# Performance work log

Measured on AMD Instinct MI355X. Metric: run time of the kernel, lower is better.

## Reference

```python
import jax, jax.numpy as jnp
import numpy as np

M, N, D = 4, 65536, 256

def setup_inputs() -> dict:
    key = jax.random.key(0)
    k1, k2, k3 = jax.random.split(key, 3)
    x = jax.random.normal(k1, (M, N, D), dtype=jnp.float32)
    # W[i,j] is the (out,in) weight of fusion_layers[i][j]; b[i,j] its bias.
    W = jax.random.normal(k2, (M, M, D, D), dtype=jnp.float32) * (1.0 / np.sqrt(D))
    b = jax.random.normal(k3, (M, M, D), dtype=jnp.float32) * 0.02
    return {"x": x, "W": W, "b": b}

def reference(x, W, b):
    # x: [M, N, D] stacked modality features (zip(*features) rows vectorized over N)
    # out[i] = x[i] + sum_{j != i} (x[j] @ W[i,j]^T + b[i,j])
    m = x.shape[0]
    mask = (1.0 - jnp.eye(m)).astype(x.dtype)            # zero on diagonal (skip i==j)
    y = jnp.einsum('ijef,jnf->ijne', W, x) + b[:, :, None, :]  # [M, M, N, D]
    out = x + jnp.einsum('ij,ijne->ine', mask, y)         # fused masked accumulation
    return out
```

## Files before the change

### kernel.cpp

```cpp
#include <hip/hip_runtime.h>
#include <hip/hip_bf16.h>
#include <stdint.h>

#define NN 65536
#define DD 256

typedef uint32_t u32;
typedef __attribute__((ext_vector_type(4))) float f32x4;
typedef __attribute__((ext_vector_type(4))) u32 u32x4;
typedef __attribute__((ext_vector_type(2))) u32 u32x2;
typedef __attribute__((ext_vector_type(8))) short s16x8;

__device__ inline unsigned short f2bf(float f) {
    union { float f; u32 u; } v; v.f = f;
    u32 u = v.u;
    return (unsigned short)((u + 0x7fffu + ((u >> 16) & 1u)) >> 16);
}

__device__ inline void gl2lds16(const void* g, void* s) {
    __builtin_amdgcn_global_load_lds(
        (const __attribute__((address_space(1))) void*)g,
        (__attribute__((address_space(3))) void*)s, 16, 0, 0);
}

__global__ void prep_w(const float* __restrict__ W, unsigned short* __restrict__ Wimg, int diag) {
    int t = blockIdx.x * blockDim.x + threadIdx.x;
    int E = t * 4;
    int tile = E >> 13;
    int pin = E & 8191;
    int col = pin >> 6;
    int r2e = pin & 63;
    int ct = tile >> 4;
    int j = (tile >> 2) & 3;
    int kk = tile & 3;
    int kl = r2e ^ ((col & 7) << 3);
    int c = ct * 128 + col;
    int i = c >> 8, e = c & 255;
    int f = kk * 64 + kl;
    u32 p0, p1;
    if (i == j) {
        unsigned short d0 = 0, d1 = 0, d2 = 0, d3 = 0;
        if (diag) {
            d0 = (e == f + 0) ? 0x3F80 : 0;
            d1 = (e == f + 1) ? 0x3F80 : 0;
            d2 = (e == f + 2) ? 0x3F80 : 0;
            d3 = (e == f + 3) ? 0x3F80 : 0;
        }
        p0 = (u32)d0 | ((u32)d1 << 16);
        p1 = (u32)d2 | ((u32)d3 << 16);
    } else {
        f32x4 w = *(const f32x4*)(W + ((size_t)((i * 4 + j) * 256 + e) << 8) + f);
        p0 = (u32)f2bf(w[0]) | ((u32)f2bf(w[1]) << 16);
        p1 = (u32)f2bf(w[2]) | ((u32)f2bf(w[3]) << 16);
    }
    u32x2 pr = {p0, p1};
    *(u32x2*)(Wimg + E) = pr;
}

__global__ void prep_x(const float* __restrict__ x, unsigned short* __restrict__ Ximg) {
    int t = blockIdx.x * blockDim.x + threadIdx.x;
    long long E = (long long)t * 4;
    int tile = (int)(E >> 14);
    int pin = (int)(E & 16383);
    int row = pin >> 6;
    int r2e = pin & 63;
    int kk = tile & 3;
    int rt = (tile >> 2) & 255;
    int j = tile >> 10;
    int kl = r2e ^ ((row & 7) << 3);
    int n = rt * 256 + row;
    int f = kk * 64 + kl;
    f32x4 v = *(const f32x4*)(x + ((size_t)j * NN + n) * DD + f);
    u32 p0 = (u32)f2bf(v[0]) | ((u32)f2bf(v[1]) << 16);
    u32 p1 = (u32)f2bf(v[2]) | ((u32)f2bf(v[3]) << 16);
    u32x2 pr = {p0, p1};
    *(u32x2*)(Ximg + E) = pr;
}

__global__ void prep_b(const float* __restrict__ b, float* __restrict__ bsum) {
    int c = blockIdx.x * blockDim.x + threadIdx.x;
    if (c >= 1024) return;
    int i = c >> 8, e = c & 255;
    float s = 0.0f;
    #pragma unroll
    for (int j = 0; j < 4; ++j)
        if (j != i) s += b[((i * 4 + j) << 8) + e];
    bsum[c] = s;
}

__global__ __launch_bounds__(512, 1) void fusion_gemm3(
    const unsigned short* __restrict__ Wimg, const unsigned short* __restrict__ Ximg,
    const float* __restrict__ bsum, float* __restrict__ out) {
    __shared__ __attribute__((aligned(16))) char lds[3][49152];

    const int tid = threadIdx.x;
    const int bid = blockIdx.x;
    const int xcd = bid & 7;
    const int slot = bid >> 3;
    const int ct = slot & 7;
    const int rhi = slot >> 3;
    const int rtile = rhi * 8 + xcd;
    const int n0 = rtile * 256;
    const int col0 = ct * 128;
    const int i = ct >> 1;
    (void)i;

    const int lane = tid & 63;
    const int wid = tid >> 6;
    const int wm = wid >> 1;
    const int wn = wid & 1;

    f32x4 acc[4][4];
    #pragma unroll
    for (int a = 0; a < 4; ++a)
        #pragma unroll
        for (int b2 = 0; b2 < 4; ++b2)
            acc[a][b2] = (f32x4){0.f, 0.f, 0.f, 0.f};

    const char* WimgB = (const char*)Wimg;
    const char* XimgB = (const char*)Ximg;
    const u32 goff = (u32)(wid * 1024 + lane * 16);
    const u32 loff = (u32)(wid * 1024);

#define STAGE(t_, bsel_)                                                              \
    {                                                                                 \
        int j_ = (t_) >> 2;                                                           \
        int kk_ = (t_) & 3;                                                           \
        const char* ab_ = XimgB + (((size_t)(j_ * 256 + rtile) * 4 + kk_) << 15) + goff; \
        char* al_ = lds[bsel_] + loff;                                                \
        _Pragma("unroll")                                                             \
        for (int q = 0; q < 4; ++q) gl2lds16(ab_ + q * 8192, al_ + q * 8192);         \
        const char* bb_ = WimgB + (((size_t)(ct * 4 + j_) * 4 + kk_) << 14) + goff;   \
        char* bl_ = lds[bsel_] + 32768 + loff;                                        \
        _Pragma("unroll")                                                             \
        for (int q = 0; q < 2; ++q) gl2lds16(bb_ + q * 8192, bl_ + q * 8192);         \
    }

#define MFMA_STEP(bsel_)                                                              \
    {                                                                                 \
        const char* Ab_ = lds[bsel_];                                                 \
        const char* Bb_ = lds[bsel_] + 32768;                                         \
        _Pragma("unroll")                                                             \
        for (int kh = 0; kh < 2; ++kh) {                                              \
            s16x8 af[4], bfr[4];                                                      \
            _Pragma("unroll")                                                         \
            for (int fm = 0; fm < 4; ++fm) {                                          \
                int row = wm * 64 + fm * 16 + (lane & 15);                            \
                u32 o = (u32)(row * 128 + kh * 64 + (lane >> 4) * 16);                \
                o ^= (u32)((row & 7) << 4);                                           \
                af[fm] = *(const s16x8*)(Ab_ + o);                                    \
            }                                                                         \
            _Pragma("unroll")                                                         \
            for (int fn = 0; fn < 4; ++fn) {                                          \
                int col = wn * 64 + fn * 16 + (lane & 15);                            \
                u32 o = (u32)(col * 128 + kh * 64 + (lane >> 4) * 16);                \
                o ^= (u32)((col & 7) << 4);                                           \
                bfr[fn] = *(const s16x8*)(Bb_ + o);                                   \
            }                                                                         \
            _Pragma("unroll")                                                         \
            for (int fm = 0; fm < 4; ++fm)                                            \
                _Pragma("unroll")                                                     \
                for (int fn = 0; fn < 4; ++fn)                                        \
                    acc[fm][fn] = __builtin_amdgcn_mfma_f32_16x16x32_bf16(            \
                        af[fm], bfr[fn], acc[fm][fn], 0, 0, 0);                       \
        }                                                                             \
    }

    STAGE(0, 0);
    STAGE(1, 1);

    #pragma unroll 1
    for (int t = 0; t < 14; ++t) {
        asm volatile("s_waitcnt vmcnt(6)" ::: "memory");
        __builtin_amdgcn_s_barrier();
        __builtin_amdgcn_sched_barrier(0);
        STAGE(t + 2, (t + 2) % 3);
        __builtin_amdgcn_s_setprio(1);
        MFMA_STEP(t % 3);
        __builtin_amdgcn_s_setprio(0);
    }
    asm volatile("s_waitcnt vmcnt(6)" ::: "memory");
    __builtin_amdgcn_s_barrier();
    __builtin_amdgcn_sched_barrier(0);
    __builtin_amdgcn_s_setprio(1);
    MFMA_STEP(2);
    __builtin_amdgcn_s_setprio(0);
    asm volatile("s_waitcnt vmcnt(0)" ::: "memory");
    __builtin_amdgcn_s_barrier();
    __builtin_amdgcn_sched_barrier(0);
    __builtin_amdgcn_s_setprio(1);
    MFMA_STEP(0);
    __builtin_amdgcn_s_setprio(0);

#undef STAGE
#undef MFMA_STEP

    const int r0 = (lane >> 4) * 4;
    const int cl = lane & 15;
    const int iout = ct >> 1;
    #pragma unroll
    for (int fm = 0; fm < 4; ++fm) {
        #pragma unroll
        for (int fn = 0; fn < 4; ++fn) {
            int col_l = wn * 64 + fn * 16 + cl;
            int cglob = col0 + col_l;
            float bs = bsum[cglob];
            int e = cglob & 255;
            #pragma unroll
            for (int r = 0; r < 4; ++r) {
                int row_l = wm * 64 + fm * 16 + r0 + r;
                int n = n0 + row_l;
                size_t oidx = ((size_t)iout * NN + n) * DD + e;
                out[oidx] = acc[fm][fn][r] + bs;
            }
        }
    }
}

__global__ __launch_bounds__(256, 2) void fusion_gemm_fb(
    const float* __restrict__ x, const unsigned short* __restrict__ Wimg,
    const float* __restrict__ bsum, float* __restrict__ out) {
    __shared__ __attribute__((aligned(16))) unsigned short Alds[128 * 64];
    __shared__ __attribute__((aligned(16))) unsigned short Blds[2][128 * 64];

    const int tid = threadIdx.x;
    const int bid = blockIdx.x;
    const int xcd = bid & 7;
    const int slot = bid >> 3;
    const int ct = slot & 7;
    const int rhi = slot >> 3;
    const int rtile = rhi * 8 + xcd;
    const int n0 = rtile * 128;
    const int col0 = ct * 128;
    const int i = ct >> 1;

    const int lane = tid & 63;
    const int wid = tid >> 6;
    const int wm = wid >> 1;
    const int wn = wid & 1;

    f32x4 acc[4][4];
    #pragma unroll
    for (int a = 0; a < 4; ++a)
        #pragma unroll
        for (int b2 = 0; b2 < 4; ++b2)
            acc[a][b2] = (f32x4){0.f, 0.f, 0.f, 0.f};

    const int sr = tid >> 1;
    const int sh = tid & 1;
    char* Ab = (char*)Alds;
    const char* WimgB = (const char*)Wimg;

    f32x4 av[8];
    {
        int j0 = (i == 0) ? 1 : 0;
        const float* asrc = x + (size_t)j0 * ((size_t)NN * DD) + (size_t)(n0 + sr) * DD + sh * 32;
        #pragma unroll
        for (int q = 0; q < 8; ++q) av[q] = *(const f32x4*)(asrc + q * 4);
        const char* base = WimgB + (((size_t)(ct * 4 + j0) * 4 + 0) << 14) + wid * 1024 + lane * 16;
        char* lb = (char*)Blds[0] + wid * 1024;
        #pragma unroll
        for (int q = 0; q < 4; ++q) gl2lds16(base + q * 4096, lb + q * 4096);
    }

    for (int t = 0; t < 12; ++t) {
        __syncthreads();
        #pragma unroll
        for (int q = 0; q < 4; ++q) {
            f32x4 v0 = av[2 * q], v1 = av[2 * q + 1];
            u32x4 p;
            p[0] = (u32)f2bf(v0[0]) | ((u32)f2bf(v0[1]) << 16);
            p[1] = (u32)f2bf(v0[2]) | ((u32)f2bf(v0[3]) << 16);
            p[2] = (u32)f2bf(v1[0]) | ((u32)f2bf(v1[1]) << 16);
            p[3] = (u32)f2bf(v1[2]) | ((u32)f2bf(v1[3]) << 16);
            u32 o = (u32)(sr * 128 + sh * 64 + q * 16);
            o ^= (u32)((sr & 7) << 4);
            *(u32x4*)(Ab + o) = p;
        }
        __syncthreads();

        if (t < 11) {
            int tn = t + 1;
            int jjn = tn >> 2;
            int jn = jjn + (jjn >= i);
            int kkn = tn & 3;
            const char* base = WimgB + (((size_t)(ct * 4 + jn) * 4 + kkn) << 14) + wid * 1024 + lane * 16;
            char* lb = (char*)Blds[tn & 1] + wid * 1024;
            #pragma unroll
            for (int q = 0; q < 4; ++q) gl2lds16(base + q * 4096, lb + q * 4096);
            const float* asrc = x + (size_t)jn * ((size_t)NN * DD) + (size_t)(n0 + sr) * DD + kkn * 64 + sh * 32;
            #pragma unroll
            for (int q = 0; q < 8; ++q) av[q] = *(const f32x4*)(asrc + q * 4);
        }

        const char* Bb = (const char*)Blds[t & 1];
        #pragma unroll
        for (int kh = 0; kh < 2; ++kh) {
            s16x8 af[4], bfr[4];
            #pragma unroll
            for (int fm = 0; fm < 4; ++fm) {
                int row = wm * 64 + fm * 16 + (lane & 15);
                u32 o = (u32)(row * 128 + kh * 64 + (lane >> 4) * 16);
                o ^= (u32)((row & 7) << 4);
                af[fm] = *(const s16x8*)(Ab + o);
            }
            #pragma unroll
            for (int fn = 0; fn < 4; ++fn) {
                int col = wn * 64 + fn * 16 + (lane & 15);
                u32 o = (u32)(col * 128 + kh * 64 + (lane >> 4) * 16);
                o ^= (u32)((col & 7) << 4);
                bfr[fn] = *(const s16x8*)(Bb + o);
            }
            #pragma unroll
            for (int fm = 0; fm < 4; ++fm)
                #pragma unroll
                for (int fn = 0; fn < 4; ++fn)
                    acc[fm][fn] = __builtin_amdgcn_mfma_f32_16x16x32_bf16(
                        af[fm], bfr[fn], acc[fm][fn], 0, 0, 0);
        }
    }

    const int r0 = (lane >> 4) * 4;
    const int cl = lane & 15;
    #pragma unroll
    for (int fm = 0; fm < 4; ++fm) {
        #pragma unroll
        for (int fn = 0; fn < 4; ++fn) {
            int col_l = wn * 64 + fn * 16 + cl;
            int cglob = col0 + col_l;
            float bs = bsum[cglob];
            int e = cglob & 255;
            #pragma unroll
            for (int r = 0; r < 4; ++r) {
                int row_l = wm * 64 + fm * 16 + r0 + r;
                int n = n0 + row_l;
                size_t oidx = ((size_t)i * NN + n) * DD + e;
                out[oidx] = acc[fm][fn][r] + x[oidx] + bs;
            }
        }
    }
}

extern "C" void kernel_launch(void* const* d_in, const int* in_sizes, int n_in,
                              void* d_out, int out_size, void* d_ws, size_t ws_size,
                              hipStream_t stream) {
    const float* x = (const float*)d_in[0];
    const float* W = (const float*)d_in[1];
    const float* b = (const float*)d_in[2];
    float* out = (float*)d_out;

    unsigned short* Wimg = (unsigned short*)d_ws;
    float* bsum = (float*)((char*)d_ws + ((size_t)2 << 20));
    const size_t ximg_off = (size_t)4 << 20;
    const size_t need = ximg_off + ((size_t)128 << 20);

    hipLaunchKernelGGL(prep_b, dim3(4), dim3(256), 0, stream, b, bsum);

    if (ws_size >= need) {
        unsigned short* Ximg = (unsigned short*)((char*)d_ws + ximg_off);
        hipLaunchKernelGGL(prep_w, dim3(1024), dim3(256), 0, stream, W, Wimg, 1);
        hipLaunchKernelGGL(prep_x, dim3(65536), dim3(256), 0, stream, x, Ximg);
        hipLaunchKernelGGL(fusion_gemm3, dim3(2048), dim3(512), 0, stream, Wimg, Ximg, bsum, out);
    } else {
        hipLaunchKernelGGL(prep_w, dim3(1024), dim3(256), 0, stream, W, Wimg, 0);
        hipLaunchKernelGGL(fusion_gemm_fb, dim3(4096), dim3(256), 0, stream, x, Wimg, bsum, out);
    }
}
```

Baseline: 262.2 us.

## Enlarge GEMM tile to 256x256 with double-buffered LDS and interleaved quadrant MFMA schedule

The main GEMM tile grows from 256x128 to 256x256 output columns per block, halving the grid and the number of times each X tile is re-read. The weight image is re-laid out to match. The triple-buffered LDS ring becomes a 2x64KB double buffer whose next-stage loads are split into four pieces and interleaved with four MFMA quadrant clusters, each guarded by barriers. Each wave now holds 128 accumulator registers, which raises register pressure, and the launch bound asks for two blocks per CU, which the 128KB of LDS may not permit.

```diff
diff --git a/kernel.cpp b/kernel.cpp
--- a/kernel.cpp
+++ b/kernel.cpp
@@ -23,7 +23,38 @@
         (__attribute__((address_space(3))) void*)s, 16, 0, 0);
 }
 
-__global__ void prep_w(const float* __restrict__ W, unsigned short* __restrict__ Wimg, int diag) {
+__global__ void prep_w256(const float* __restrict__ W, unsigned short* __restrict__ Wimg) {
+    int t = blockIdx.x * blockDim.x + threadIdx.x;
+    int E = t * 4;
+    int tile = E >> 14;
+    int pin = E & 16383;
+    int col = pin >> 6;
+    int r2e = pin & 63;
+    int ct = tile >> 4;
+    int j = (tile >> 2) & 3;
+    int kk = tile & 3;
+    int kl = r2e ^ ((col & 7) << 3);
+    int i = ct;
+    int e = col;
+    int f = kk * 64 + kl;
+    u32 p0, p1;
+    if (i == j) {
+        unsigned short d0 = (e == f + 0) ? 0x3F80 : 0;
+        unsigned short d1 = (e == f + 1) ? 0x3F80 : 0;
+        unsigned short d2 = (e == f + 2) ? 0x3F80 : 0;
+        unsigned short d3 = (e == f + 3) ? 0x3F80 : 0;
+        p0 = (u32)d0 | ((u32)d1 << 16);
+        p1 = (u32)d2 | ((u32)d3 << 16);
+    } else {
+        f32x4 w = *(const f32x4*)(W + ((size_t)((i * 4 + j) * 256 + e) << 8) + f);
+        p0 = (u32)f2bf(w[0]) | ((u32)f2bf(w[1]) << 16);
+        p1 = (u32)f2bf(w[2]) | ((u32)f2bf(w[3]) << 16);
+    }
+    u32x2 pr = {p0, p1};
+    *(u32x2*)(Wimg + E) = pr;
+}
+
+__global__ void prep_w128(const float* __restrict__ W, unsigned short* __restrict__ Wimg) {
     int t = blockIdx.x * blockDim.x + threadIdx.x;
     int E = t * 4;
     int tile = E >> 13;
@@ -39,15 +70,7 @@
     int f = kk * 64 + kl;
     u32 p0, p1;
     if (i == j) {
-        unsigned short d0 = 0, d1 = 0, d2 = 0, d3 = 0;
-        if (diag) {
-            d0 = (e == f + 0) ? 0x3F80 : 0;
-            d1 = (e == f + 1) ? 0x3F80 : 0;
-            d2 = (e == f + 2) ? 0x3F80 : 0;
-            d3 = (e == f + 3) ? 0x3F80 : 0;
-        }
-        p0 = (u32)d0 | ((u32)d1 << 16);
-        p1 = (u32)d2 | ((u32)d3 << 16);
+        p0 = 0u; p1 = 0u;
     } else {
         f32x4 w = *(const f32x4*)(W + ((size_t)((i * 4 + j) * 256 + e) << 8) + f);
         p0 = (u32)f2bf(w[0]) | ((u32)f2bf(w[1]) << 16);
@@ -88,130 +111,161 @@
     bsum[c] = s;
 }
 
-__global__ __launch_bounds__(512, 1) void fusion_gemm3(
+__global__ __launch_bounds__(512, 2) void fusion_gemm4(
     const unsigned short* __restrict__ Wimg, const unsigned short* __restrict__ Ximg,
     const float* __restrict__ bsum, float* __restrict__ out) {
-    __shared__ __attribute__((aligned(16))) char lds[3][49152];
+    __shared__ __attribute__((aligned(16))) char lds[2][65536];
 
     const int tid = threadIdx.x;
     const int bid = blockIdx.x;
     const int xcd = bid & 7;
     const int slot = bid >> 3;
-    const int ct = slot & 7;
-    const int rhi = slot >> 3;
+    const int ct = slot & 3;
+    const int rhi = slot >> 2;
     const int rtile = rhi * 8 + xcd;
     const int n0 = rtile * 256;
-    const int col0 = ct * 128;
-    const int i = ct >> 1;
-    (void)i;
+    const int col0 = ct * 256;
 
     const int lane = tid & 63;
     const int wid = tid >> 6;
-    const int wm = wid >> 1;
-    const int wn = wid & 1;
-
-    f32x4 acc[4][4];
+    const int wm = wid & 1;
+    const int wn = wid >> 1;
+
+    f32x4 acc[8][4];
     #pragma unroll
-    for (int a = 0; a < 4; ++a)
+    for (int a = 0; a < 8; ++a)
         #pragma unroll
         for (int b2 = 0; b2 < 4; ++b2)
             acc[a][b2] = (f32x4){0.f, 0.f, 0.f, 0.f};
 
     const char* WimgB = (const char*)Wimg;
     const char* XimgB = (const char*)Ximg;
+    const u32 loff = (u32)(wid * 1024);
     const u32 goff = (u32)(wid * 1024 + lane * 16);
-    const u32 loff = (u32)(wid * 1024);
-
-#define STAGE(t_, bsel_)                                                              \
+
+    s16x8 af[2][4];
+    s16x8 bf2[2][2];
+
+#define STAGE_PAIR(t_, q_)                                                            \
     {                                                                                 \
         int j_ = (t_) >> 2;                                                           \
         int kk_ = (t_) & 3;                                                           \
-        const char* ab_ = XimgB + (((size_t)(j_ * 256 + rtile) * 4 + kk_) << 15) + goff; \
-        char* al_ = lds[bsel_] + loff;                                                \
+        const char* as_ = XimgB + (((size_t)((j_ * 256 + rtile) * 4 + kk_)) << 15)    \
+                          + (q_) * 8192 + goff;                                       \
+        gl2lds16(as_, ldsN + (q_) * 8192 + loff);                                     \
+        const char* bs_ = WimgB + (((size_t)((ct * 4 + j_) * 4 + kk_)) << 15)         \
+                          + (q_) * 8192 + goff;                                       \
+        gl2lds16(bs_, ldsN + 32768 + (q_) * 8192 + loff);                             \
+    }
+
+#define RD_A(mh_)                                                                     \
+    _Pragma("unroll")                                                                 \
+    for (int kh = 0; kh < 2; ++kh) {                                                  \
         _Pragma("unroll")                                                             \
-        for (int q = 0; q < 4; ++q) gl2lds16(ab_ + q * 8192, al_ + q * 8192);         \
-        const char* bb_ = WimgB + (((size_t)(ct * 4 + j_) * 4 + kk_) << 14) + goff;   \
-        char* bl_ = lds[bsel_] + 32768 + loff;                                        \
+        for (int fm = 0; fm < 4; ++fm) {                                              \
+            int r_ = wm * 128 + ((mh_) * 4 + fm) * 16 + (lane & 15);                  \
+            u32 o_ = (u32)(r_ * 128 + kh * 64 + (lane >> 4) * 16);                    \
+            o_ ^= (u32)((r_ & 7) << 4);                                               \
+            af[kh][fm] = *(const s16x8*)(Ab + o_);                                    \
+        }                                                                             \
+    }
+
+#define RD_B(nh_)                                                                     \
+    _Pragma("unroll")                                                                 \
+    for (int kh = 0; kh < 2; ++kh) {                                                  \
         _Pragma("unroll")                                                             \
-        for (int q = 0; q < 2; ++q) gl2lds16(bb_ + q * 8192, bl_ + q * 8192);         \
-    }
-
-#define MFMA_STEP(bsel_)                                                              \
-    {                                                                                 \
-        const char* Ab_ = lds[bsel_];                                                 \
-        const char* Bb_ = lds[bsel_] + 32768;                                         \
+        for (int fn = 0; fn < 2; ++fn) {                                              \
+            int c_ = wn * 64 + ((nh_) * 2 + fn) * 16 + (lane & 15);                   \
+            u32 o_ = (u32)(c_ * 128 + kh * 64 + (lane >> 4) * 16);                    \
+            o_ ^= (u32)((c_ & 7) << 4);                                               \
+            bf2[kh][fn] = *(const s16x8*)(Bb + o_);                                   \
+        }                                                                             \
+    }
+
+#define MM_Q(mh_, nh_)                                                                \
+    _Pragma("unroll")                                                                 \
+    for (int kh = 0; kh < 2; ++kh) {                                                  \
         _Pragma("unroll")                                                             \
-        for (int kh = 0; kh < 2; ++kh) {                                              \
-            s16x8 af[4], bfr[4];                                                      \
+        for (int fm = 0; fm < 4; ++fm) {                                              \
             _Pragma("unroll")                                                         \
-            for (int fm = 0; fm < 4; ++fm) {                                          \
-                int row = wm * 64 + fm * 16 + (lane & 15);                            \
-                u32 o = (u32)(row * 128 + kh * 64 + (lane >> 4) * 16);                \
-                o ^= (u32)((row & 7) << 4);                                           \
-                af[fm] = *(const s16x8*)(Ab_ + o);                                    \
+            for (int fn = 0; fn < 2; ++fn) {                                          \
+                acc[(mh_) * 4 + fm][(nh_) * 2 + fn] =                                 \
+                    __builtin_amdgcn_mfma_f32_16x16x32_bf16(                          \
+                        af[kh][fm], bf2[kh][fn],                                      \
+                        acc[(mh_) * 4 + fm][(nh_) * 2 + fn], 0, 0, 0);                \
             }                                                                         \
-            _Pragma("unroll")                                                         \
-            for (int fn = 0; fn < 4; ++fn) {                                          \
-                int col = wn * 64 + fn * 16 + (lane & 15);                            \
-                u32 o = (u32)(col * 128 + kh * 64 + (lane >> 4) * 16);                \
-                o ^= (u32)((col & 7) << 4);                                           \
-                bfr[fn] = *(const s16x8*)(Bb_ + o);                                   \
-            }                                                                         \
-            _Pragma("unroll")                                                         \
-            for (int fm = 0; fm < 4; ++fm)                                            \
-                _Pragma("unroll")                                                     \
-                for (int fn = 0; fn < 4; ++fn)                                        \
-                    acc[fm][fn] = __builtin_amdgcn_mfma_f32_16x16x32_bf16(            \
-                        af[fm], bfr[fn], acc[fm][fn], 0, 0, 0);                       \
         }                                                                             \
     }
 
-    STAGE(0, 0);
-    STAGE(1, 1);
+#define MFMA_CLUSTER(mh_, nh_)                                                        \
+    __builtin_amdgcn_sched_barrier(0);                                                \
+    __builtin_amdgcn_s_barrier();                                                     \
+    __builtin_amdgcn_sched_barrier(0);                                                \
+    __builtin_amdgcn_s_setprio(1);                                                    \
+    MM_Q(mh_, nh_);                                                                   \
+    __builtin_amdgcn_s_setprio(0);                                                    \
+    __builtin_amdgcn_sched_barrier(0);                                                \
+    __builtin_amdgcn_s_barrier();
+
+    {
+        char* ldsN = lds[0];
+        STAGE_PAIR(0, 0);
+        STAGE_PAIR(0, 1);
+        STAGE_PAIR(0, 2);
+        STAGE_PAIR(0, 3);
+    }
 
     #pragma unroll 1
-    for (int t = 0; t < 14; ++t) {
-        asm volatile("s_waitcnt vmcnt(6)" ::: "memory");
+    for (int t = 0; t < 16; ++t) {
+        const char* Ab = lds[t & 1];
+        const char* Bb = Ab + 32768;
+        char* ldsN = lds[(t + 1) & 1];
+
+        if (t < 15) {
+            STAGE_PAIR(t + 1, 0);
+            asm volatile("s_waitcnt vmcnt(2)" ::: "memory");
+        } else {
+            asm volatile("s_waitcnt vmcnt(0)" ::: "memory");
+        }
         __builtin_amdgcn_s_barrier();
         __builtin_amdgcn_sched_barrier(0);
-        STAGE(t + 2, (t + 2) % 3);
-        __builtin_amdgcn_s_setprio(1);
-        MFMA_STEP(t % 3);
-        __builtin_amdgcn_s_setprio(0);
-    }
-    asm volatile("s_waitcnt vmcnt(6)" ::: "memory");
-    __builtin_amdgcn_s_barrier();
-    __builtin_amdgcn_sched_barrier(0);
-    __builtin_amdgcn_s_setprio(1);
-    MFMA_STEP(2);
-    __builtin_amdgcn_s_setprio(0);
-    asm volatile("s_waitcnt vmcnt(0)" ::: "memory");
-    __builtin_amdgcn_s_barrier();
-    __builtin_amdgcn_sched_barrier(0);
-    __builtin_amdgcn_s_setprio(1);
-    MFMA_STEP(0);
-    __builtin_amdgcn_s_setprio(0);
-
-#undef STAGE
-#undef MFMA_STEP
+
+        RD_A(0);
+        RD_B(0);
+        if (t < 15) STAGE_PAIR(t + 1, 1);
+        MFMA_CLUSTER(0, 0);
+
+        RD_B(1);
+        if (t < 15) STAGE_PAIR(t + 1, 2);
+        MFMA_CLUSTER(0, 1);
+
+        RD_A(1);
+        if (t < 15) STAGE_PAIR(t + 1, 3);
+        MFMA_CLUSTER(1, 1);
+
+        RD_B(0);
+        MFMA_CLUSTER(1, 0);
+    }
+
+#undef STAGE_PAIR
+#undef RD_A
+#undef RD_B
+#undef MM_Q
+#undef MFMA_CLUSTER
 
     const int r0 = (lane >> 4) * 4;
     const int cl = lane & 15;
-    const int iout = ct >> 1;
     #pragma unroll
-    for (int fm = 0; fm < 4; ++fm) {
-        #pragma unroll
-        for (int fn = 0; fn < 4; ++fn) {
-            int col_l = wn * 64 + fn * 16 + cl;
-            int cglob = col0 + col_l;
-            float bs = bsum[cglob];
-            int e = cglob & 255;
+    for (int mf = 0; mf < 8; ++mf) {
+        #pragma unroll
+        for (int nf = 0; nf < 4; ++nf) {
+            int col_l = wn * 64 + nf * 16 + cl;
+            float bs = bsum[col0 + col_l];
             #pragma unroll
             for (int r = 0; r < 4; ++r) {
-                int row_l = wm * 64 + fm * 16 + r0 + r;
-                int n = n0 + row_l;
-                size_t oidx = ((size_t)iout * NN + n) * DD + e;
-                out[oidx] = acc[fm][fn][r] + bs;
+                int n = n0 + wm * 128 + mf * 16 + r0 + r;
+                size_t oidx = ((size_t)ct * NN + n) * DD + col_l;
+                out[oidx] = acc[mf][nf][r] + bs;
             }
         }
     }
@@ -358,11 +412,11 @@
 
     if (ws_size >= need) {
         unsigned short* Ximg = (unsigned short*)((char*)d_ws + ximg_off);
-        hipLaunchKernelGGL(prep_w, dim3(1024), dim3(256), 0, stream, W, Wimg, 1);
+        hipLaunchKernelGGL(prep_w256, dim3(1024), dim3(256), 0, stream, W, Wimg);
         hipLaunchKernelGGL(prep_x, dim3(65536), dim3(256), 0, stream, x, Ximg);
-        hipLaunchKernelGGL(fusion_gemm3, dim3(2048), dim3(512), 0, stream, Wimg, Ximg, bsum, out);
+        hipLaunchKernelGGL(fusion_gemm4, dim3(1024), dim3(512), 0, stream, Wimg, Ximg, bsum, out);
     } else {
-        hipLaunchKernelGGL(prep_w, dim3(1024), dim3(256), 0, stream, W, Wimg, 0);
+        hipLaunchKernelGGL(prep_w128, dim3(1024), dim3(256), 0, stream, W, Wimg);
         hipLaunchKernelGGL(fusion_gemm_fb, dim3(4096), dim3(256), 0, stream, x, Wimg, bsum, out);
     }
 }
```

New measurement: 267.1 us. Within noise of the previous version (+1.9%).
